# Kernel tuning notes

Hardware: AMD Instinct MI355X
Metric: run time of the kernel (lower is better)

Reference implementation:

```python
import jax, jax.numpy as jnp
import numpy as np

D_MODEL = 1024
N_HEADS = 16
RANK = 128
N_COMPRESS = 16
N_KNOWLEDGE = 32768
KNOWLEDGE_K = 8
B, S = 4, 1024
EPS = 1e-5


def setup_inputs() -> dict:
    key = jax.random.key(0)
    ks = jax.random.split(key, 16)
    inp = {
        'x': jax.random.normal(ks[0], (B, S, D_MODEL), jnp.float32),
        'mask': jnp.tril(jnp.ones((S, S), bool))[None, None],  # causal [1,1,S,S]
        'compress_neurons': jax.random.normal(ks[1], (N_COMPRESS, D_MODEL, RANK), jnp.float32) / np.sqrt(D_MODEL),
        'knowledge_K': jax.random.normal(ks[2], (N_KNOWLEDGE, RANK), jnp.float32) * 0.02,
        'knowledge_V': jax.random.normal(ks[3], (N_KNOWLEDGE, D_MODEL), jnp.float32) * 0.02,
        'router_Q': jax.random.normal(ks[4], (D_MODEL, N_COMPRESS), jnp.float32) * 0.02,
        'router_K': jax.random.normal(ks[5], (D_MODEL, N_COMPRESS), jnp.float32) * 0.02,
        'router_V': jax.random.normal(ks[6], (D_MODEL, N_COMPRESS), jnp.float32) * 0.02,
        'router_M': jax.random.normal(ks[7], (D_MODEL, N_COMPRESS), jnp.float32) * 0.02,
        'W_Q': jax.random.normal(ks[8], (RANK, D_MODEL), jnp.float32) / np.sqrt(RANK),
        'W_K': jax.random.normal(ks[9], (RANK, D_MODEL), jnp.float32) / np.sqrt(RANK),
        'W_V': jax.random.normal(ks[10], (RANK, D_MODEL), jnp.float32) / np.sqrt(RANK),
        'W_O': jax.random.normal(ks[11], (D_MODEL, D_MODEL), jnp.float32) / np.sqrt(D_MODEL),
        'ln1_g': jnp.ones((D_MODEL,), jnp.float32),
        'ln1_b': jnp.zeros((D_MODEL,), jnp.float32),
        'ln2_g': jnp.ones((D_MODEL,), jnp.float32),
        'ln2_b': jnp.zeros((D_MODEL,), jnp.float32),
    }
    return inp


def _layernorm(x, g, b):
    mu = x.mean(-1, keepdims=True)
    var = ((x - mu) ** 2).mean(-1, keepdims=True)
    return (x - mu) * jax.lax.rsqrt(var + EPS) * g + b


def _compress(x, router_W, neurons):
    # x: [B,S,D]; router_W: [D,N]; neurons: [N,D,R]
    weights = jax.nn.softmax(x @ router_W, axis=-1)               # [B,S,N]
    all_proj = jnp.einsum('bsd,ndr->bsnr', x, neurons)            # [B,S,N,R]
    return jnp.einsum('bsnr,bsn->bsr', all_proj, weights)         # [B,S,R]


def reference(x, mask, compress_neurons, knowledge_K, knowledge_V,
              router_Q, router_K, router_V, router_M,
              W_Q, W_K, W_V, W_O, ln1_g, ln1_b, ln2_g, ln2_b):
    d_head = D_MODEL // N_HEADS
    h = _layernorm(x, ln1_g, ln1_b)
    # soft-routed low-rank compression for Q/K/V
    hQ = _compress(h, router_Q, compress_neurons)
    hK = _compress(h, router_K, compress_neurons)
    hV = _compress(h, router_V, compress_neurons)
    Q = (hQ @ W_Q).reshape(B, S, N_HEADS, d_head).transpose(0, 2, 1, 3)
    K = (hK @ W_K).reshape(B, S, N_HEADS, d_head).transpose(0, 2, 1, 3)
    V = (hV @ W_V).reshape(B, S, N_HEADS, d_head).transpose(0, 2, 1, 3)
    scores = jnp.einsum('bhqd,bhkd->bhqk', Q, K) / np.sqrt(d_head)
    scores = jnp.where(mask, scores, -jnp.inf)
    attn = jax.nn.softmax(scores, axis=-1)
    attn_out = jnp.einsum('bhqk,bhkd->bhqd', attn, V)
    attn_out = attn_out.transpose(0, 2, 1, 3).reshape(B, S, D_MODEL)
    x = x + attn_out @ W_O
    # knowledge memory
    h2 = _layernorm(x, ln2_g, ln2_b)
    Qm = _compress(h2, router_M, compress_neurons)                # [B,S,R]
    kscores = Qm @ knowledge_K.T / np.sqrt(RANK)                  # [B,S,NK]
    topk_scores, topk_idx = jax.lax.top_k(kscores, KNOWLEDGE_K)
    kweights = jax.nn.softmax(topk_scores, axis=-1)               # [B,S,k]
    selected_V = knowledge_V[topk_idx]                            # [B,S,k,D]
    mem_out = jnp.einsum('bskd,bsk->bsd', selected_V, kweights)
    return x + mem_out
```

## Files before the change

kernel.cpp:

```cpp
#include <hip/hip_runtime.h>
#include <math.h>

#define DM     1024
#define RANK   128
#define NCMP   16
#define NKNOW  32768
#define TOPK   8
#define NROWS  4096
#define NEG_BIG -3.0e38f
#define TK_SPLIT 32
#define TK_KEYS (NKNOW / TK_SPLIT)

typedef __attribute__((ext_vector_type(8))) short s8v;
typedef __attribute__((ext_vector_type(4))) float f4v;

__device__ __forceinline__ unsigned short f2bf(float f) {
  union { float fl; unsigned u; } v; v.fl = f;
  return (unsigned short)((v.u + 0x7FFFu + ((v.u >> 16) & 1u)) >> 16);
}
__device__ __forceinline__ float bf2f(unsigned short u) {
  return __uint_as_float((unsigned)u << 16);
}
__device__ __forceinline__ f4v mfma16(s8v a, s8v b, f4v c) {
  return __builtin_amdgcn_mfma_f32_16x16x32_bf16(a, b, c, 0, 0, 0);
}
__device__ __forceinline__ unsigned umed3(unsigned a, unsigned b, unsigned c) {
  unsigned d;
  asm("v_med3_u32 %0, %1, %2, %3" : "=v"(d) : "v"(a), "v"(b), "v"(c));
  return d;
}
__device__ __forceinline__ void gload16(const unsigned short* g, unsigned short* l) {
  __builtin_amdgcn_global_load_lds(
      (const __attribute__((address_space(1))) unsigned int*)(g),
      (__attribute__((address_space(3))) unsigned int*)(l), 16, 0, 0);
}
#define VMCNT(n) asm volatile("s_waitcnt vmcnt(" #n ")" ::: "memory")
#define BAR() __builtin_amdgcn_s_barrier()

__global__ __launch_bounds__(256) void ln_router3_kernel(const float* __restrict__ x,
                                                         const float* __restrict__ g,
                                                         const float* __restrict__ b,
                                                         unsigned short* __restrict__ obf,
                                                         const float* __restrict__ R0,
                                                         const float* __restrict__ R1,
                                                         const float* __restrict__ R2,
                                                         float* __restrict__ w0,
                                                         float* __restrict__ w1,
                                                         float* __restrict__ w2) {
  __shared__ float hs[DM];
  __shared__ float red[3][16][17];
  __shared__ float red1[4], red2[4];
  const int row = blockIdx.x, t = threadIdx.x;
  const float4 v = reinterpret_cast<const float4*>(x + (size_t)row * DM)[t];
  float s = v.x + v.y + v.z + v.w;
#pragma unroll
  for (int m = 1; m <= 32; m <<= 1) s += __shfl_xor(s, m);
  if ((t & 63) == 0) red1[t >> 6] = s;
  __syncthreads();
  const float mu = (red1[0] + red1[1] + red1[2] + red1[3]) * (1.0f / DM);
  const float dx = v.x - mu, dy = v.y - mu, dz = v.z - mu, dw = v.w - mu;
  float ss = dx * dx + dy * dy + dz * dz + dw * dw;
#pragma unroll
  for (int m = 1; m <= 32; m <<= 1) ss += __shfl_xor(ss, m);
  if ((t & 63) == 0) red2[t >> 6] = ss;
  __syncthreads();
  const float var = (red2[0] + red2[1] + red2[2] + red2[3]) * (1.0f / DM);
  const float inv = rsqrtf(var + 1e-5f);
  const float4 g4 = reinterpret_cast<const float4*>(g)[t];
  const float4 b4 = reinterpret_cast<const float4*>(b)[t];
  const float h0 = dx * inv * g4.x + b4.x, h1 = dy * inv * g4.y + b4.y;
  const float h2 = dz * inv * g4.z + b4.z, h3 = dw * inv * g4.w + b4.w;
  reinterpret_cast<ushort4*>(obf + (size_t)row * DM)[t] =
      make_ushort4(f2bf(h0), f2bf(h1), f2bf(h2), f2bf(h3));
  hs[t * 4 + 0] = h0; hs[t * 4 + 1] = h1; hs[t * 4 + 2] = h2; hs[t * 4 + 3] = h3;
  __syncthreads();
  const int o = t & 15, seg = t >> 4;
  float a0 = 0.f, a1 = 0.f, a2 = 0.f;
  for (int d = seg * 64; d < seg * 64 + 64; ++d) {
    const float hv = hs[d];
    a0 += hv * R0[d * NCMP + o];
    a1 += hv * R1[d * NCMP + o];
    a2 += hv * R2[d * NCMP + o];
  }
  red[0][seg][o] = a0; red[1][seg][o] = a1; red[2][seg][o] = a2;
  __syncthreads();
  if (t < 48) {
    const int gg = t >> 4, oo = t & 15;
    float dot = 0.f;
#pragma unroll
    for (int s2 = 0; s2 < 16; ++s2) dot += red[gg][s2][oo];
    float m = dot;
#pragma unroll
    for (int msk = 1; msk < 16; msk <<= 1) m = fmaxf(m, __shfl_xor(m, msk));
    const float e = __expf(dot - m);
    float ssum = e;
#pragma unroll
    for (int msk = 1; msk < 16; msk <<= 1) ssum += __shfl_xor(ssum, msk);
    float* wp = (gg == 0) ? w0 : (gg == 1) ? w1 : w2;
    wp[(size_t)row * NCMP + oo] = e / ssum;
  }
}

__global__ __launch_bounds__(256) void ln_router1_kernel(const float* __restrict__ x,
                                                         const float* __restrict__ g,
                                                         const float* __restrict__ b,
                                                         unsigned short* __restrict__ obf,
                                                         const float* __restrict__ R,
                                                         float* __restrict__ w) {
  __shared__ float hs[DM];
  __shared__ float red[16][17];
  __shared__ float red1[4], red2[4];
  const int row = blockIdx.x, t = threadIdx.x;
  const float4 v = reinterpret_cast<const float4*>(x + (size_t)row * DM)[t];
  float s = v.x + v.y + v.z + v.w;
#pragma unroll
  for (int m = 1; m <= 32; m <<= 1) s += __shfl_xor(s, m);
  if ((t & 63) == 0) red1[t >> 6] = s;
  __syncthreads();
  const float mu = (red1[0] + red1[1] + red1[2] + red1[3]) * (1.0f / DM);
  const float dx = v.x - mu, dy = v.y - mu, dz = v.z - mu, dw = v.w - mu;
  float ss = dx * dx + dy * dy + dz * dz + dw * dw;
#pragma unroll
  for (int m = 1; m <= 32; m <<= 1) ss += __shfl_xor(ss, m);
  if ((t & 63) == 0) red2[t >> 6] = ss;
  __syncthreads();
  const float var = (red2[0] + red2[1] + red2[2] + red2[3]) * (1.0f / DM);
  const float inv = rsqrtf(var + 1e-5f);
  const float4 g4 = reinterpret_cast<const float4*>(g)[t];
  const float4 b4 = reinterpret_cast<const float4*>(b)[t];
  const float h0 = dx * inv * g4.x + b4.x, h1 = dy * inv * g4.y + b4.y;
  const float h2 = dz * inv * g4.z + b4.z, h3 = dw * inv * g4.w + b4.w;
  reinterpret_cast<ushort4*>(obf + (size_t)row * DM)[t] =
      make_ushort4(f2bf(h0), f2bf(h1), f2bf(h2), f2bf(h3));
  hs[t * 4 + 0] = h0; hs[t * 4 + 1] = h1; hs[t * 4 + 2] = h2; hs[t * 4 + 3] = h3;
  __syncthreads();
  const int o = t & 15, seg = t >> 4;
  float acc = 0.f;
  for (int d = seg * 64; d < seg * 64 + 64; ++d) acc += hs[d] * R[d * NCMP + o];
  red[seg][o] = acc;
  __syncthreads();
  if (t < 16) {
    float dot = 0.f;
#pragma unroll
    for (int s2 = 0; s2 < 16; ++s2) dot += red[s2][t];
    float m = dot;
#pragma unroll
    for (int msk = 1; msk < 16; msk <<= 1) m = fmaxf(m, __shfl_xor(m, msk));
    const float e = __expf(dot - m);
    float ssum = e;
#pragma unroll
    for (int msk = 1; msk < 16; msk <<= 1) ssum += __shfl_xor(ssum, msk);
    w[(size_t)row * NCMP + t] = e / ssum;
  }
}

__device__ __forceinline__ void tcvt_body(const float* __restrict__ in,
                                          unsigned short* __restrict__ out,
                                          int K, int N, int bx, int by, int bz, int t) {
  __shared__ float ld[32][33];
  const int k0 = by * 32, n0 = bx * 32;
  const float* ib = in + (size_t)bz * K * N;
  unsigned short* ob = out + (size_t)bz * K * N;
  const int kl = t >> 3, nl = (t & 7) * 4;
  const float4 v = *reinterpret_cast<const float4*>(&ib[(size_t)(k0 + kl) * N + n0 + nl]);
  ld[kl][nl] = v.x; ld[kl][nl + 1] = v.y; ld[kl][nl + 2] = v.z; ld[kl][nl + 3] = v.w;
  __syncthreads();
  const int nw = t >> 3, kw = (t & 7) * 4;
  ushort4 o = make_ushort4(f2bf(ld[kw][nw]), f2bf(ld[kw + 1][nw]),
                           f2bf(ld[kw + 2][nw]), f2bf(ld[kw + 3][nw]));
  *reinterpret_cast<ushort4*>(&ob[(size_t)(n0 + nw) * K + k0 + kw]) = o;
}

__global__ __launch_bounds__(256) void prep_kernel(const float* __restrict__ kK,
                                                   unsigned short* __restrict__ kKb,
                                                   const float* __restrict__ neur,
                                                   unsigned short* __restrict__ neurT,
                                                   const float* __restrict__ WQ,
                                                   const float* __restrict__ WK,
                                                   const float* __restrict__ WV,
                                                   unsigned short* __restrict__ WQKVt,
                                                   const float* __restrict__ WO,
                                                   unsigned short* __restrict__ WOt) {
  const int bid = blockIdx.x, t = threadIdx.x;
  if (bid < 2048) {
    const int i = bid * 256 + t;
    const float4 a = reinterpret_cast<const float4*>(kK)[2 * i];
    const float4 b = reinterpret_cast<const float4*>(kK)[2 * i + 1];
    reinterpret_cast<ushort4*>(kKb)[2 * i] =
        make_ushort4(f2bf(a.x), f2bf(a.y), f2bf(a.z), f2bf(a.w));
    reinterpret_cast<ushort4*>(kKb)[2 * i + 1] =
        make_ushort4(f2bf(b.x), f2bf(b.y), f2bf(b.z), f2bf(b.w));
  } else if (bid < 4096) {
    const int lb = bid - 2048;
    tcvt_body(neur, neurT, DM, RANK, lb & 3, (lb >> 2) & 31, lb >> 7, t);
  } else if (bid < 4224) {
    const int lb = bid - 4096;
    tcvt_body(WQ, WQKVt, RANK, DM, lb & 31, lb >> 5, 0, t);
  } else if (bid < 4352) {
    const int lb = bid - 4224;
    tcvt_body(WK, WQKVt + (size_t)DM * RANK, RANK, DM, lb & 31, lb >> 5, 0, t);
  } else if (bid < 4480) {
    const int lb = bid - 4352;
    tcvt_body(WV, WQKVt + (size_t)2 * DM * RANK, RANK, DM, lb & 31, lb >> 5, 0, t);
  } else {
    const int lb = bid - 4480;
    tcvt_body(WO, WOt, DM, DM, lb & 31, lb >> 5, 0, t);
  }
}

__global__ __launch_bounds__(256) void vtr_kernel(const unsigned short* __restrict__ V,
                                                  unsigned short* __restrict__ Vt) {
  __shared__ unsigned short ld[32][40];
  const int bh = blockIdx.z, b = bh >> 4, hh = bh & 15;
  const int s0 = blockIdx.x * 32, d0 = blockIdx.y * 32;
  const int t = threadIdx.x;
  const int r = t >> 3, c = (t & 7) * 4;
  *reinterpret_cast<ushort4*>(&ld[r][c]) =
      *reinterpret_cast<const ushort4*>(&V[(size_t)(b * 1024 + s0 + r) * DM + hh * 64 + d0 + c]);
  __syncthreads();
  ushort4 o;
  o.x = ld[c + 0][r]; o.y = ld[c + 1][r]; o.z = ld[c + 2][r]; o.w = ld[c + 3][r];
  *reinterpret_cast<ushort4*>(&Vt[((size_t)bh * 64 + d0 + r) * 1024 + s0 + c]) = o;
}

template <bool OUT_BF16, bool RES>
__global__ __launch_bounds__(256) void mfma_nt(const unsigned short* __restrict__ A,
                                               const unsigned short* __restrict__ B,
                                               float* __restrict__ Cf,
                                               unsigned short* __restrict__ Cb,
                                               const float* __restrict__ res,
                                               int M, int N, int K, int bshift) {
  __shared__ unsigned short As[2][128 * 64];
  __shared__ unsigned short Bs[2][128 * 64];
  const int t = threadIdx.x;
  const int lane = t & 63, w = t >> 6;
  const int wm = w >> 1, wn = w & 1;
  const int bm = blockIdx.y, bn = blockIdx.x;
  const int l15 = lane & 15, l4 = lane >> 4;
  f4v acc[4][4] = {};
  const int srow = w * 32 + (lane >> 3);
  const int scol = ((lane & 7) ^ (lane >> 3)) * 8;
  const unsigned short* ga = A + (size_t)(bm * 128 + srow) * K + scol;
  const unsigned short* gb = B + (size_t)(bm >> bshift) * ((size_t)N * K) +
                             (size_t)(bn * 128 + srow) * K + scol;
  const int NITER = K >> 6;
#pragma unroll
  for (int j = 0; j < 4; ++j) {
    gload16(ga + (size_t)j * 8 * K, &As[0][w * 2048 + j * 512]);
    gload16(gb + (size_t)j * 8 * K, &Bs[0][w * 2048 + j * 512]);
  }
  for (int it = 0; it < NITER; ++it) {
    const int cur = it & 1;
    if (it + 1 < NITER) {
      const int k0 = (it + 1) * 64;
      unsigned short* const nA = &As[cur ^ 1][w * 2048];
      unsigned short* const nB = &Bs[cur ^ 1][w * 2048];
#pragma unroll
      for (int j = 0; j < 4; ++j) {
        gload16(ga + (size_t)j * 8 * K + k0, nA + j * 512);
        gload16(gb + (size_t)j * 8 * K + k0, nB + j * 512);
      }
      VMCNT(8);
    } else {
      VMCNT(0);
    }
    BAR();
#pragma unroll
    for (int ks = 0; ks < 2; ++ks) {
      s8v af[4], bf[4];
      const int sc = (ks * 32 + l4 * 8) ^ ((l15 & 7) * 8);
#pragma unroll
      for (int i = 0; i < 4; ++i) {
        af[i] = *reinterpret_cast<const s8v*>(&As[cur][(wm * 64 + i * 16 + l15) * 64 + sc]);
        bf[i] = *reinterpret_cast<const s8v*>(&Bs[cur][(wn * 64 + i * 16 + l15) * 64 + sc]);
      }
#pragma unroll
      for (int i = 0; i < 4; ++i)
#pragma unroll
        for (int j = 0; j < 4; ++j) acc[i][j] = mfma16(af[i], bf[j], acc[i][j]);
    }
    BAR();
  }
#pragma unroll
  for (int i = 0; i < 4; ++i) {
#pragma unroll
    for (int j = 0; j < 4; ++j) {
#pragma unroll
      for (int r = 0; r < 4; ++r) {
        const int row = bm * 128 + wm * 64 + i * 16 + l4 * 4 + r;
        const int col = bn * 128 + wn * 64 + j * 16 + l15;
        float v = acc[i][j][r];
        if constexpr (RES) v += res[(size_t)row * N + col];
        if constexpr (OUT_BF16) Cb[(size_t)row * N + col] = f2bf(v);
        else Cf[(size_t)row * N + col] = v;
      }
    }
  }
}

__global__ __launch_bounds__(128) void wsum_kernel(const unsigned short* __restrict__ ap,
                                                   const float* __restrict__ w0,
                                                   const float* __restrict__ w1,
                                                   const float* __restrict__ w2,
                                                   unsigned short* __restrict__ o0,
                                                   unsigned short* __restrict__ o1,
                                                   unsigned short* __restrict__ o2,
                                                   float scale) {
  const int row = blockIdx.x, r = threadIdx.x;
  float wa[16], wb[16], wc[16];
#pragma unroll
  for (int n = 0; n < 16; ++n) wa[n] = w0[(size_t)row * NCMP + n];
  if (w1) {
#pragma unroll
    for (int n = 0; n < 16; ++n) wb[n] = w1[(size_t)row * NCMP + n];
  }
  if (w2) {
#pragma unroll
    for (int n = 0; n < 16; ++n) wc[n] = w2[(size_t)row * NCMP + n];
  }
  float a0 = 0.f, a1 = 0.f, a2 = 0.f;
  const unsigned short* apr = ap + (size_t)row * (NCMP * RANK) + r;
#pragma unroll
  for (int n = 0; n < 16; ++n) {
    const float v = bf2f(apr[n * RANK]);
    a0 += v * wa[n];
    if (w1) a1 += v * wb[n];
    if (w2) a2 += v * wc[n];
  }
  o0[(size_t)row * RANK + r] = f2bf(a0 * scale);
  if (o1) o1[(size_t)row * RANK + r] = f2bf(a1 * scale);
  if (o2) o2[(size_t)row * RANK + r] = f2bf(a2 * scale);
}

__global__ __launch_bounds__(256) void flash_kernel(const unsigned short* __restrict__ Q,
                                                    const unsigned short* __restrict__ K,
                                                    const unsigned short* __restrict__ Vt,
                                                    unsigned short* __restrict__ O) {
  __shared__ unsigned short Qs[8 * 512];
  __shared__ unsigned short Ks[2][8 * 512];
  __shared__ unsigned short Vs[2][8 * 512];
  __shared__ unsigned short Ps[64 * 72];
  const int bh = blockIdx.x, qt = blockIdx.y;
  const int b = bh >> 4, hh = bh & 15;
  const int base = b * 1024, q0 = qt * 64, col = hh * 64;
  const int t = threadIdx.x;
  const int lane = t & 63, w = t >> 6;
  const int l15 = lane & 15, l4 = lane >> 4;
  const unsigned short* Vh = Vt + (size_t)bh * 64 * 1024;
#pragma unroll
  for (int j = 0; j < 2; ++j)
    gload16(&Q[(size_t)(base + q0 + w * 16 + l15) * DM + col + j * 32 + l4 * 8],
            Qs + (2 * w + j) * 512);
#pragma unroll
  for (int j = 0; j < 2; ++j) {
    gload16(&K[(size_t)(base + w * 16 + l15) * DM + col + j * 32 + l4 * 8],
            Ks[0] + (2 * w + j) * 512);
    gload16(&Vh[(size_t)(w * 16 + l15) * 1024 + j * 32 + l4 * 8],
            Vs[0] + (2 * w + j) * 512);
  }
  float m_r[4], l_r[4];
  f4v o[4] = {};
#pragma unroll
  for (int r = 0; r < 4; ++r) { m_r[r] = NEG_BIG; l_r[r] = 0.f; }
  for (int kt = 0; kt <= qt; ++kt) {
    const int cur = kt & 1;
    if (kt < qt) {
      const int kn = (kt + 1) * 64;
#pragma unroll
      for (int j = 0; j < 2; ++j) {
        gload16(&K[(size_t)(base + kn + w * 16 + l15) * DM + col + j * 32 + l4 * 8],
                Ks[cur ^ 1] + (2 * w + j) * 512);
        gload16(&Vh[(size_t)(w * 16 + l15) * 1024 + kn + j * 32 + l4 * 8],
                Vs[cur ^ 1] + (2 * w + j) * 512);
      }
      VMCNT(4);
    } else {
      VMCNT(0);
    }
    BAR();
    const int k0 = kt * 64;
    f4v s[4] = {};
#pragma unroll
    for (int ks = 0; ks < 2; ++ks) {
      s8v a = *reinterpret_cast<const s8v*>(&Qs[(2 * w + ks) * 512 + lane * 8]);
#pragma unroll
      for (int nj = 0; nj < 4; ++nj) {
        s8v bb = *reinterpret_cast<const s8v*>(&Ks[cur][(2 * nj + ks) * 512 + lane * 8]);
        s[nj] = mfma16(a, bb, s[nj]);
      }
    }
#pragma unroll
    for (int r = 0; r < 4; ++r) {
      const int grow = q0 + w * 16 + l4 * 4 + r;
      float sv[4];
#pragma unroll
      for (int nj = 0; nj < 4; ++nj) {
        const float xx = s[nj][r] * 0.125f;
        const int gcol = k0 + nj * 16 + l15;
        sv[nj] = (gcol <= grow) ? xx : NEG_BIG;
      }
      float mt = fmaxf(fmaxf(sv[0], sv[1]), fmaxf(sv[2], sv[3]));
#pragma unroll
      for (int msk = 1; msk < 16; msk <<= 1) mt = fmaxf(mt, __shfl_xor(mt, msk));
      const float mn = fmaxf(m_r[r], mt);
      const float sc = __expf(m_r[r] - mn);
      m_r[r] = mn;
      float rs = 0.f, pv[4];
#pragma unroll
      for (int nj = 0; nj < 4; ++nj) { pv[nj] = __expf(sv[nj] - mn); rs += pv[nj]; }
#pragma unroll
      for (int msk = 1; msk < 16; msk <<= 1) rs += __shfl_xor(rs, msk);
      l_r[r] = l_r[r] * sc + rs;
#pragma unroll
      for (int nd = 0; nd < 4; ++nd) o[nd][r] *= sc;
#pragma unroll
      for (int nj = 0; nj < 4; ++nj)
        Ps[(w * 16 + l4 * 4 + r) * 72 + nj * 16 + l15] = f2bf(pv[nj]);
    }
#pragma unroll
    for (int ks = 0; ks < 2; ++ks) {
      s8v pa = *reinterpret_cast<const s8v*>(&Ps[(w * 16 + l15) * 72 + ks * 32 + l4 * 8]);
#pragma unroll
      for (int nd = 0; nd < 4; ++nd) {
        s8v vb = *reinterpret_cast<const s8v*>(&Vs[cur][(2 * nd + ks) * 512 + lane * 8]);
        o[nd] = mfma16(pa, vb, o[nd]);
      }
    }
    BAR();
  }
#pragma unroll
  for (int nd = 0; nd < 4; ++nd)
#pragma unroll
    for (int r = 0; r < 4; ++r) {
      const int grow = base + q0 + w * 16 + l4 * 4 + r;
      O[(size_t)grow * DM + col + nd * 16 + l15] = f2bf(o[nd][r] / l_r[r]);
    }
}

__global__ __launch_bounds__(256) void topk_kernel(const unsigned short* __restrict__ Qm,
                                                   const unsigned short* __restrict__ kK,
                                                   float* __restrict__ tks,
                                                   int* __restrict__ tki) {
  __shared__ __align__(16) char arena[32768];
  unsigned short* const K0 = (unsigned short*)arena;
  unsigned short* const K1 = (unsigned short*)(arena + 8192);
  unsigned short* const K2 = (unsigned short*)(arena + 16384);
  unsigned short* const K3 = (unsigned short*)(arena + 24576);
  const int id = blockIdx.x;
  const int sp = (id & 7) * 4 + ((id >> 3) & 3);
  const int rb = id >> 5;
  const int r0 = rb * 64, kb0 = sp * TK_KEYS;
  const int t = threadIdx.x;
  const int lane = t & 63, w = t >> 6;
  const int l15 = lane & 15, l4 = lane >> 4;
  s8v qf[4];
#pragma unroll
  for (int ks = 0; ks < 4; ++ks)
    qf[ks] = *reinterpret_cast<const s8v*>(
        &Qm[(size_t)(r0 + w * 16 + l15) * RANK + ks * 32 + l4 * 8]);
  unsigned bs0 = 0u, bs1 = 0u, bs2 = 0u, bs3 = 0u, bs4 = 0u, bs5 = 0u, bs6 = 0u, bs7 = 0u;
  const int s0i = 2 * w, s1i = 2 * w + 1;
  const unsigned short* g0 = kK + (size_t)(kb0 + (s0i >> 2) * 16 + l15) * RANK + (s0i & 3) * 32 + l4 * 8;
  const unsigned short* g1 = kK + (size_t)(kb0 + (s1i >> 2) * 16 + l15) * RANK + (s1i & 3) * 32 + l4 * 8;
  gload16(g0, K0 + s0i * 512);
  gload16(g1, K0 + s1i * 512);

#define TK_STEP(BC, BN, CH)                                                        \
  {                                                                                \
    if ((CH) + 1 < 32) {                                                           \
      const size_t off_ = (size_t)((CH) + 1) * 32 * RANK;                          \
      gload16(g0 + off_, (BN) + s0i * 512);                                        \
      gload16(g1 + off_, (BN) + s1i * 512);                                        \
      VMCNT(2);                                                                    \
    } else {                                                                       \
      VMCNT(0);                                                                    \
    }                                                                              \
    BAR();                                                                         \
    f4v a0_ = f4v{4.f, 4.f, 4.f, 4.f};                                             \
    f4v a1_ = f4v{4.f, 4.f, 4.f, 4.f};                                             \
    __builtin_amdgcn_s_setprio(1);                                                 \
    _Pragma("unroll")                                                              \
    for (int ks_ = 0; ks_ < 4; ++ks_) {                                            \
      a0_ = mfma16(*reinterpret_cast<const s8v*>(&(BC)[ks_ * 512 + lane * 8]),     \
                   qf[ks_], a0_);                                                  \
      a1_ = mfma16(*reinterpret_cast<const s8v*>(&(BC)[(4 + ks_) * 512 + lane * 8]),\
                   qf[ks_], a1_);                                                  \
    }                                                                              \
    __builtin_amdgcn_s_setprio(0);                                                 \
    const unsigned ivb_ = 2047u - (unsigned)((CH) * 32 + l4 * 4);                  \
    _Pragma("unroll")                                                              \
    for (int r_ = 0; r_ < 4; ++r_) {                                               \
      const unsigned u_ = __float_as_uint(a0_[r_]);                                \
      const unsigned pk_ = (u_ & 0xFFFFF800u) | (ivb_ - (unsigned)r_);             \
      bs7 = umed3(bs6, pk_, bs7); bs6 = umed3(bs5, pk_, bs6);                      \
      bs5 = umed3(bs4, pk_, bs5); bs4 = umed3(bs3, pk_, bs4);                      \
      bs3 = umed3(bs2, pk_, bs3); bs2 = umed3(bs1, pk_, bs2);                      \
      bs1 = umed3(bs0, pk_, bs1); bs0 = max(bs0, pk_);                             \
    }                                                                              \
    _Pragma("unroll")                                                              \
    for (int r_ = 0; r_ < 4; ++r_) {                                               \
      const unsigned u_ = __float_as_uint(a1_[r_]);                                \
      const unsigned pk_ = (u_ & 0xFFFFF800u) | (ivb_ - (unsigned)(16 + r_));      \
      bs7 = umed3(bs6, pk_, bs7); bs6 = umed3(bs5, pk_, bs6);                      \
      bs5 = umed3(bs4, pk_, bs5); bs4 = umed3(bs3, pk_, bs4);                      \
      bs3 = umed3(bs2, pk_, bs3); bs2 = umed3(bs1, pk_, bs2);                      \
      bs1 = umed3(bs0, pk_, bs1); bs0 = max(bs0, pk_);                             \
    }                                                                              \
  }

  for (int c4 = 0; c4 < 32; c4 += 4) {
    TK_STEP(K0, K1, c4 + 0);
    TK_STEP(K1, K2, c4 + 1);
    TK_STEP(K2, K3, c4 + 2);
    TK_STEP(K3, K0, c4 + 3);
  }
#undef TK_STEP

  unsigned* const M = (unsigned*)arena;
  const int row = w * 16 + l15;
  {
    unsigned* mp = M + row * 33 + l4 * 8;
    mp[0] = bs0; mp[1] = bs1; mp[2] = bs2; mp[3] = bs3;
    mp[4] = bs4; mp[5] = bs5; mp[6] = bs6; mp[7] = bs7;
  }
  __syncthreads();
  if (t < 64) {
    const unsigned* mr = M + t * 33;
    int h0 = 0, h1 = 0, h2 = 0, h3 = 0;
    const size_t oo = ((size_t)sp * NROWS + r0 + t) * TOPK;
    for (int k = 0; k < TOPK; ++k) {
      const unsigned c0 = (h0 < 8) ? mr[0 + h0] : 0u;
      const unsigned c1 = (h1 < 8) ? mr[8 + h1] : 0u;
      const unsigned c2 = (h2 < 8) ? mr[16 + h2] : 0u;
      const unsigned c3 = (h3 < 8) ? mr[24 + h3] : 0u;
      const unsigned m01 = (c0 >= c1) ? c0 : c1; const int l01 = (c0 >= c1) ? 0 : 1;
      const unsigned m23 = (c2 >= c3) ? c2 : c3; const int l23 = (c2 >= c3) ? 2 : 3;
      const unsigned bst = (m01 >= m23) ? m01 : m23;
      const int bl = (m01 >= m23) ? l01 : l23;
      tks[oo + k] = __uint_as_float(bst & 0xFFFFF800u) - 4.0f;
      tki[oo + k] = kb0 + 2047 - (int)(bst & 0x7FFu);
      h0 += (bl == 0); h1 += (bl == 1); h2 += (bl == 2); h3 += (bl == 3);
    }
  }
}

__global__ __launch_bounds__(256) void gather_kernel(const float* __restrict__ tks,
                                                     const int* __restrict__ tki,
                                                     const float* __restrict__ kV,
                                                     float* __restrict__ out) {
  __shared__ float ls[TK_SPLIT * TOPK];
  __shared__ int li[TK_SPLIT * TOPK];
  __shared__ float selv[TOPK];
  __shared__ int seli[TOPK];
  __shared__ float wsel[TOPK];
  const int row = blockIdx.x, t = threadIdx.x;
  if (t < TK_SPLIT * TOPK) {
    const int l = t >> 3, k = t & 7;
    ls[t] = tks[((size_t)l * NROWS + row) * TOPK + k];
    li[t] = tki[((size_t)l * NROWS + row) * TOPK + k];
  }
  __syncthreads();
  if (t < TK_SPLIT * TOPK) {
    const float v = ls[t];
    const int myid = li[t];
    int rank = 0;
    for (int j = 0; j < TK_SPLIT * TOPK; ++j) {
      const float u = ls[j];
      rank += (u > v) || (u == v && li[j] < myid);
    }
    if (rank < TOPK) { selv[rank] = v; seli[rank] = myid; }
  }
  __syncthreads();
  if (t == 0) {
    const float m = selv[0];
    float sum = 0.f, e[TOPK];
#pragma unroll
    for (int k = 0; k < TOPK; ++k) { e[k] = __expf(selv[k] - m); sum += e[k]; }
    const float inv = 1.f / sum;
#pragma unroll
    for (int k = 0; k < TOPK; ++k) wsel[k] = e[k] * inv;
  }
  __syncthreads();
  float4 accv = reinterpret_cast<float4*>(out + (size_t)row * DM)[t];
#pragma unroll
  for (int k = 0; k < TOPK; ++k) {
    const float4 v4 = reinterpret_cast<const float4*>(kV + (size_t)seli[k] * DM)[t];
    const float wk = wsel[k];
    accv.x += wk * v4.x; accv.y += wk * v4.y; accv.z += wk * v4.z; accv.w += wk * v4.w;
  }
  reinterpret_cast<float4*>(out + (size_t)row * DM)[t] = accv;
}

extern "C" void kernel_launch(void* const* d_in, const int* in_sizes, int n_in,
                              void* d_out, int out_size, void* d_ws, size_t ws_size,
                              hipStream_t stream) {
  (void)in_sizes; (void)n_in; (void)out_size; (void)ws_size;
  const float* x    = (const float*)d_in[0];
  const float* neur = (const float*)d_in[2];
  const float* kK   = (const float*)d_in[3];
  const float* kV   = (const float*)d_in[4];
  const float* rQ   = (const float*)d_in[5];
  const float* rK   = (const float*)d_in[6];
  const float* rV   = (const float*)d_in[7];
  const float* rM   = (const float*)d_in[8];
  const float* WQ   = (const float*)d_in[9];
  const float* WK   = (const float*)d_in[10];
  const float* WV   = (const float*)d_in[11];
  const float* WO   = (const float*)d_in[12];
  const float* g1   = (const float*)d_in[13];
  const float* b1   = (const float*)d_in[14];
  const float* g2   = (const float*)d_in[15];
  const float* b2   = (const float*)d_in[16];
  float* out = (float*)d_out;

  char* base = (char*)d_ws;
  auto alloc = [&](size_t bytes) { char* r = base; base += (bytes + 255) & ~(size_t)255; return r; };
  unsigned short* hbf   = (unsigned short*)alloc((size_t)NROWS * DM * 2);
  unsigned short* apb   = (unsigned short*)alloc((size_t)3 * NROWS * DM * 2);
  unsigned short* neurT = (unsigned short*)alloc((size_t)NCMP * RANK * DM * 2);
  unsigned short* WQKVt = (unsigned short*)alloc((size_t)3 * DM * RANK * 2);
  unsigned short* WOt   = (unsigned short*)alloc((size_t)DM * DM * 2);
  unsigned short* kKb   = (unsigned short*)alloc((size_t)NKNOW * RANK * 2);
  unsigned short* hQKVb = (unsigned short*)alloc((size_t)3 * NROWS * RANK * 2);
  unsigned short* Qmb   = (unsigned short*)alloc((size_t)NROWS * RANK * 2);
  unsigned short* Vtb   = (unsigned short*)alloc((size_t)NROWS * DM * 2);
  float* wQw = (float*)alloc((size_t)NROWS * NCMP * 4);
  float* wKw = (float*)alloc((size_t)NROWS * NCMP * 4);
  float* wVw = (float*)alloc((size_t)NROWS * NCMP * 4);
  float* wMw = (float*)alloc((size_t)NROWS * NCMP * 4);
  float* tks = (float*)alloc((size_t)TK_SPLIT * NROWS * TOPK * 4);
  int*   tki = (int*)alloc((size_t)TK_SPLIT * NROWS * TOPK * 4);
  unsigned short* Qb = apb;
  unsigned short* Kb = Qb + (size_t)NROWS * DM;
  unsigned short* Vb = Kb + (size_t)NROWS * DM;
  unsigned short* attnb = hbf;
  unsigned short* hQb = hQKVb;
  unsigned short* hKb = hQKVb + (size_t)NROWS * RANK;
  unsigned short* hVb = hQKVb + (size_t)2 * NROWS * RANK;

  prep_kernel<<<5504, 256, 0, stream>>>(kK, kKb, neur, neurT, WQ, WK, WV, WQKVt, WO, WOt);

  ln_router3_kernel<<<NROWS, 256, 0, stream>>>(x, g1, b1, hbf, rQ, rK, rV, wQw, wKw, wVw);
  mfma_nt<true, false><<<dim3(16, 32), 256, 0, stream>>>(hbf, neurT, nullptr, apb, nullptr,
                                                         NROWS, NCMP * RANK, DM, 30);
  wsum_kernel<<<NROWS, 128, 0, stream>>>(apb, wQw, wKw, wVw, hQb, hKb, hVb, 1.0f);
  mfma_nt<true, false><<<dim3(8, 96), 256, 0, stream>>>(hQKVb, WQKVt, nullptr, Qb, nullptr,
                                                        3 * NROWS, DM, RANK, 5);
  vtr_kernel<<<dim3(32, 2, 64), 256, 0, stream>>>(Vb, Vtb);
  flash_kernel<<<dim3(64, 16), 256, 0, stream>>>(Qb, Kb, Vtb, attnb);
  mfma_nt<false, true><<<dim3(8, 32), 256, 0, stream>>>(attnb, WOt, out, nullptr, x,
                                                        NROWS, DM, DM, 30);

  ln_router1_kernel<<<NROWS, 256, 0, stream>>>(out, g2, b2, hbf, rM, wMw);
  mfma_nt<true, false><<<dim3(16, 32), 256, 0, stream>>>(hbf, neurT, nullptr, apb, nullptr,
                                                         NROWS, NCMP * RANK, DM, 30);
  wsum_kernel<<<NROWS, 128, 0, stream>>>(apb, wMw, nullptr, nullptr, Qmb, nullptr, nullptr,
                                         0.08838834764831845f );
  topk_kernel<<<2048, 256, 0, stream>>>(Qmb, kKb, tks, tki);
  gather_kernel<<<NROWS, 256, 0, stream>>>(tks, tki, kV, out);
}
```

Before: 353.0 us.

## Move router logits from scalar LayerNorm loop to MFMA GEMM plus softmax kernel

Splits the fused LayerNorm+router kernels into a plain LayerNorm that writes bf16, a bf16 MFMA GEMM computing all four router logit sets at once against a transposed, zero-padded router matrix built in prep, and a small softmax kernel. The aim is to replace the per-row scalar FP32 dot-product loop, which re-reads the router weights from global memory for every row, with matrix-core work. The cost is two extra launches per LayerNorm, a scores buffer round-trip through memory, and bf16 rounding of router inputs and weights, which may change softmax weights slightly.

```diff
diff --git a/kernel.cpp b/kernel.cpp
--- a/kernel.cpp
+++ b/kernel.cpp
@@ -37,18 +37,10 @@
 #define VMCNT(n) asm volatile("s_waitcnt vmcnt(" #n ")" ::: "memory")
 #define BAR() __builtin_amdgcn_s_barrier()
 
-__global__ __launch_bounds__(256) void ln_router3_kernel(const float* __restrict__ x,
-                                                         const float* __restrict__ g,
-                                                         const float* __restrict__ b,
-                                                         unsigned short* __restrict__ obf,
-                                                         const float* __restrict__ R0,
-                                                         const float* __restrict__ R1,
-                                                         const float* __restrict__ R2,
-                                                         float* __restrict__ w0,
-                                                         float* __restrict__ w1,
-                                                         float* __restrict__ w2) {
-  __shared__ float hs[DM];
-  __shared__ float red[3][16][17];
+__global__ __launch_bounds__(256) void ln_kernel(const float* __restrict__ x,
+                                                 const float* __restrict__ g,
+                                                 const float* __restrict__ b,
+                                                 unsigned short* __restrict__ obf) {
   __shared__ float red1[4], red2[4];
   const int row = blockIdx.x, t = threadIdx.x;
   const float4 v = reinterpret_cast<const float4*>(x + (size_t)row * DM)[t];
@@ -68,90 +60,28 @@
   const float inv = rsqrtf(var + 1e-5f);
   const float4 g4 = reinterpret_cast<const float4*>(g)[t];
   const float4 b4 = reinterpret_cast<const float4*>(b)[t];
-  const float h0 = dx * inv * g4.x + b4.x, h1 = dy * inv * g4.y + b4.y;
-  const float h2 = dz * inv * g4.z + b4.z, h3 = dw * inv * g4.w + b4.w;
-  reinterpret_cast<ushort4*>(obf + (size_t)row * DM)[t] =
-      make_ushort4(f2bf(h0), f2bf(h1), f2bf(h2), f2bf(h3));
-  hs[t * 4 + 0] = h0; hs[t * 4 + 1] = h1; hs[t * 4 + 2] = h2; hs[t * 4 + 3] = h3;
-  __syncthreads();
-  const int o = t & 15, seg = t >> 4;
-  float a0 = 0.f, a1 = 0.f, a2 = 0.f;
-  for (int d = seg * 64; d < seg * 64 + 64; ++d) {
-    const float hv = hs[d];
-    a0 += hv * R0[d * NCMP + o];
-    a1 += hv * R1[d * NCMP + o];
-    a2 += hv * R2[d * NCMP + o];
-  }
-  red[0][seg][o] = a0; red[1][seg][o] = a1; red[2][seg][o] = a2;
-  __syncthreads();
-  if (t < 48) {
-    const int gg = t >> 4, oo = t & 15;
-    float dot = 0.f;
-#pragma unroll
-    for (int s2 = 0; s2 < 16; ++s2) dot += red[gg][s2][oo];
-    float m = dot;
-#pragma unroll
-    for (int msk = 1; msk < 16; msk <<= 1) m = fmaxf(m, __shfl_xor(m, msk));
-    const float e = __expf(dot - m);
-    float ssum = e;
-#pragma unroll
-    for (int msk = 1; msk < 16; msk <<= 1) ssum += __shfl_xor(ssum, msk);
-    float* wp = (gg == 0) ? w0 : (gg == 1) ? w1 : w2;
-    wp[(size_t)row * NCMP + oo] = e / ssum;
-  }
-}
-
-__global__ __launch_bounds__(256) void ln_router1_kernel(const float* __restrict__ x,
-                                                         const float* __restrict__ g,
-                                                         const float* __restrict__ b,
-                                                         unsigned short* __restrict__ obf,
-                                                         const float* __restrict__ R,
-                                                         float* __restrict__ w) {
-  __shared__ float hs[DM];
-  __shared__ float red[16][17];
-  __shared__ float red1[4], red2[4];
+  ushort4 u = make_ushort4(f2bf(dx * inv * g4.x + b4.x), f2bf(dy * inv * g4.y + b4.y),
+                           f2bf(dz * inv * g4.z + b4.z), f2bf(dw * inv * g4.w + b4.w));
+  reinterpret_cast<ushort4*>(obf + (size_t)row * DM)[t] = u;
+}
+
+__global__ __launch_bounds__(64) void softmax16_kernel(const float* __restrict__ scores,
+                                                       float* __restrict__ w0,
+                                                       float* __restrict__ w1,
+                                                       float* __restrict__ w2,
+                                                       float* __restrict__ w3) {
   const int row = blockIdx.x, t = threadIdx.x;
-  const float4 v = reinterpret_cast<const float4*>(x + (size_t)row * DM)[t];
-  float s = v.x + v.y + v.z + v.w;
-#pragma unroll
-  for (int m = 1; m <= 32; m <<= 1) s += __shfl_xor(s, m);
-  if ((t & 63) == 0) red1[t >> 6] = s;
-  __syncthreads();
-  const float mu = (red1[0] + red1[1] + red1[2] + red1[3]) * (1.0f / DM);
-  const float dx = v.x - mu, dy = v.y - mu, dz = v.z - mu, dw = v.w - mu;
-  float ss = dx * dx + dy * dy + dz * dz + dw * dw;
-#pragma unroll
-  for (int m = 1; m <= 32; m <<= 1) ss += __shfl_xor(ss, m);
-  if ((t & 63) == 0) red2[t >> 6] = ss;
-  __syncthreads();
-  const float var = (red2[0] + red2[1] + red2[2] + red2[3]) * (1.0f / DM);
-  const float inv = rsqrtf(var + 1e-5f);
-  const float4 g4 = reinterpret_cast<const float4*>(g)[t];
-  const float4 b4 = reinterpret_cast<const float4*>(b)[t];
-  const float h0 = dx * inv * g4.x + b4.x, h1 = dy * inv * g4.y + b4.y;
-  const float h2 = dz * inv * g4.z + b4.z, h3 = dw * inv * g4.w + b4.w;
-  reinterpret_cast<ushort4*>(obf + (size_t)row * DM)[t] =
-      make_ushort4(f2bf(h0), f2bf(h1), f2bf(h2), f2bf(h3));
-  hs[t * 4 + 0] = h0; hs[t * 4 + 1] = h1; hs[t * 4 + 2] = h2; hs[t * 4 + 3] = h3;
-  __syncthreads();
-  const int o = t & 15, seg = t >> 4;
-  float acc = 0.f;
-  for (int d = seg * 64; d < seg * 64 + 64; ++d) acc += hs[d] * R[d * NCMP + o];
-  red[seg][o] = acc;
-  __syncthreads();
-  if (t < 16) {
-    float dot = 0.f;
-#pragma unroll
-    for (int s2 = 0; s2 < 16; ++s2) dot += red[s2][t];
-    float m = dot;
-#pragma unroll
-    for (int msk = 1; msk < 16; msk <<= 1) m = fmaxf(m, __shfl_xor(m, msk));
-    const float e = __expf(dot - m);
-    float ssum = e;
-#pragma unroll
-    for (int msk = 1; msk < 16; msk <<= 1) ssum += __shfl_xor(ssum, msk);
-    w[(size_t)row * NCMP + t] = e / ssum;
-  }
+  const int g = t >> 4, o = t & 15;
+  const float v = scores[(size_t)row * 128 + g * 16 + o];
+  float m = v;
+#pragma unroll
+  for (int msk = 1; msk < 16; msk <<= 1) m = fmaxf(m, __shfl_xor(m, msk));
+  const float e = __expf(v - m);
+  float s = e;
+#pragma unroll
+  for (int msk = 1; msk < 16; msk <<= 1) s += __shfl_xor(s, msk);
+  float* wp = (g == 0) ? w0 : (g == 1) ? w1 : (g == 2) ? w2 : w3;
+  if (wp) wp[(size_t)row * NCMP + o] = e / s;
 }
 
 __device__ __forceinline__ void tcvt_body(const float* __restrict__ in,
@@ -180,7 +110,12 @@
                                                    const float* __restrict__ WV,
                                                    unsigned short* __restrict__ WQKVt,
                                                    const float* __restrict__ WO,
-                                                   unsigned short* __restrict__ WOt) {
+                                                   unsigned short* __restrict__ WOt,
+                                                   const float* __restrict__ rQ,
+                                                   const float* __restrict__ rK,
+                                                   const float* __restrict__ rV,
+                                                   const float* __restrict__ rM,
+                                                   unsigned short* __restrict__ rTb) {
   const int bid = blockIdx.x, t = threadIdx.x;
   if (bid < 2048) {
     const int i = bid * 256 + t;
@@ -202,9 +137,20 @@
   } else if (bid < 4480) {
     const int lb = bid - 4352;
     tcvt_body(WV, WQKVt + (size_t)2 * DM * RANK, RANK, DM, lb & 31, lb >> 5, 0, t);
-  } else {
+  } else if (bid < 5504) {
     const int lb = bid - 4480;
     tcvt_body(WO, WOt, DM, DM, lb & 31, lb >> 5, 0, t);
+  } else if (bid < 5520) {
+    const int lb = bid - 5504;
+    const int m = lb >> 2, chunk = lb & 3;
+    const float* Rm = (m == 0) ? rQ : (m == 1) ? rK : (m == 2) ? rV : rM;
+    const int d = chunk * 256 + t;
+#pragma unroll
+    for (int j = 0; j < 16; ++j)
+      rTb[(size_t)(m * 16 + j) * DM + d] = f2bf(Rm[d * NCMP + j]);
+  } else {
+    const int idx = (bid - 5520) * 256 + t;
+    reinterpret_cast<ushort4*>(rTb + (size_t)64 * DM)[idx] = make_ushort4(0, 0, 0, 0);
   }
 }
 
@@ -621,9 +567,11 @@
   unsigned short* WQKVt = (unsigned short*)alloc((size_t)3 * DM * RANK * 2);
   unsigned short* WOt   = (unsigned short*)alloc((size_t)DM * DM * 2);
   unsigned short* kKb   = (unsigned short*)alloc((size_t)NKNOW * RANK * 2);
+  unsigned short* rTb   = (unsigned short*)alloc((size_t)128 * DM * 2);
   unsigned short* hQKVb = (unsigned short*)alloc((size_t)3 * NROWS * RANK * 2);
   unsigned short* Qmb   = (unsigned short*)alloc((size_t)NROWS * RANK * 2);
   unsigned short* Vtb   = (unsigned short*)alloc((size_t)NROWS * DM * 2);
+  float* scores = (float*)alloc((size_t)NROWS * 128 * 4);
   float* wQw = (float*)alloc((size_t)NROWS * NCMP * 4);
   float* wKw = (float*)alloc((size_t)NROWS * NCMP * 4);
   float* wVw = (float*)alloc((size_t)NROWS * NCMP * 4);
@@ -638,11 +586,15 @@
   unsigned short* hKb = hQKVb + (size_t)NROWS * RANK;
   unsigned short* hVb = hQKVb + (size_t)2 * NROWS * RANK;
 
-  prep_kernel<<<5504, 256, 0, stream>>>(kK, kKb, neur, neurT, WQ, WK, WV, WQKVt, WO, WOt);
-
-  ln_router3_kernel<<<NROWS, 256, 0, stream>>>(x, g1, b1, hbf, rQ, rK, rV, wQw, wKw, wVw);
+  prep_kernel<<<5584, 256, 0, stream>>>(kK, kKb, neur, neurT, WQ, WK, WV, WQKVt, WO, WOt,
+                                        rQ, rK, rV, rM, rTb);
+
+  ln_kernel<<<NROWS, 256, 0, stream>>>(x, g1, b1, hbf);
   mfma_nt<true, false><<<dim3(16, 32), 256, 0, stream>>>(hbf, neurT, nullptr, apb, nullptr,
                                                          NROWS, NCMP * RANK, DM, 30);
+  mfma_nt<false, false><<<dim3(1, 32), 256, 0, stream>>>(hbf, rTb, scores, nullptr, nullptr,
+                                                         NROWS, 128, DM, 30);
+  softmax16_kernel<<<NROWS, 64, 0, stream>>>(scores, wQw, wKw, wVw, nullptr);
   wsum_kernel<<<NROWS, 128, 0, stream>>>(apb, wQw, wKw, wVw, hQb, hKb, hVb, 1.0f);
   mfma_nt<true, false><<<dim3(8, 96), 256, 0, stream>>>(hQKVb, WQKVt, nullptr, Qb, nullptr,
                                                         3 * NROWS, DM, RANK, 5);
@@ -651,9 +603,12 @@
   mfma_nt<false, true><<<dim3(8, 32), 256, 0, stream>>>(attnb, WOt, out, nullptr, x,
                                                         NROWS, DM, DM, 30);
 
-  ln_router1_kernel<<<NROWS, 256, 0, stream>>>(out, g2, b2, hbf, rM, wMw);
+  ln_kernel<<<NROWS, 256, 0, stream>>>(out, g2, b2, hbf);
   mfma_nt<true, false><<<dim3(16, 32), 256, 0, stream>>>(hbf, neurT, nullptr, apb, nullptr,
                                                          NROWS, NCMP * RANK, DM, 30);
+  mfma_nt<false, false><<<dim3(1, 32), 256, 0, stream>>>(hbf, rTb, scores, nullptr, nullptr,
+                                                         NROWS, 128, DM, 30);
+  softmax16_kernel<<<NROWS, 64, 0, stream>>>(scores, nullptr, nullptr, nullptr, wMw);
   wsum_kernel<<<NROWS, 128, 0, stream>>>(apb, wMw, nullptr, nullptr, Qmb, nullptr, nullptr,
                                          0.08838834764831845f );
   topk_kernel<<<2048, 256, 0, stream>>>(Qmb, kKb, tks, tki);
```

New measurement: 312.2 us. 11.6% less time.
